# Optimization experiments

Hardware: AMD Instinct MI355X
Metric: run time of the kernel (lower is better)

The kernel has to match this reference:

```python
import jax, jax.numpy as jnp
import numpy as np

HEADS = 8
DIM_HEAD = 64
SCALE = DIM_HEAD ** -0.5


def setup_inputs() -> dict:
    key = jax.random.key(0)
    ks = jax.random.split(key, 6)
    b, n, dim, inner = 8, 1024, 512, HEADS * DIM_HEAD
    return {
        "x": jax.random.normal(ks[0], (b, n, dim), jnp.float32),
        "y": jax.random.normal(ks[1], (b, n, dim), jnp.float32),
        "wq": jax.random.normal(ks[2], (dim, inner), jnp.float32) * 0.02,
        "wkv": jax.random.normal(ks[3], (dim, 2 * inner), jnp.float32) * 0.02,
        "wout": jax.random.normal(ks[4], (inner, dim), jnp.float32) * 0.02,
        "bout": jnp.zeros((dim,), jnp.float32),
    }


def _split_heads(t):
    # [b, n, h*d] -> [b, h, n, d]
    b, n, hd = t.shape
    return t.reshape(b, n, HEADS, DIM_HEAD).transpose(0, 2, 1, 3)


def _merge_heads(t):
    # [b, h, n, d] -> [b, n, h*d]
    b, h, n, d = t.shape
    return t.transpose(0, 2, 1, 3).reshape(b, n, h * d)


def _cross_attn(q_in, kv_in, wq, wkv, wout, bout):
    # queries from q_in, keys/values from kv_in; top-(nk//4) masked softmax attention
    nk = kv_in.shape[1]
    q = _split_heads(q_in @ wq)                     # [b,h,nq,d]
    kv = kv_in @ wkv                                # [b,nk,2*inner]
    k, v = jnp.split(kv, 2, axis=-1)
    k, v = _split_heads(k), _split_heads(v)         # [b,h,nk,d]
    dots = jnp.einsum('bhid,bhjd->bhij', q, k) * SCALE  # [b,h,nq,nk]
    kk = max(nk // 4, 1)
    kth = jax.lax.top_k(dots, kk)[0][..., -1:]      # k-th largest per row
    masked = jnp.where(dots >= kth, dots, -jnp.inf)
    attn = jax.nn.softmax(masked, axis=-1)
    out = jnp.einsum('bhij,bhjd->bhid', attn, v)
    return _merge_heads(out) @ wout + bout


def reference(x, y, wq, wkv, wout, bout):
    out_y = _cross_attn(y, x, wq, wkv, wout, bout)  # y attends to x
    out_x = _cross_attn(x, y, wq, wkv, wout, bout)  # x attends to y
    return (out_x, out_y)
```

## Files before the change

### kernel.cpp

```cpp
#include <hip/hip_runtime.h>
#include <hip/hip_bf16.h>

typedef __attribute__((ext_vector_type(8))) short bfx8;
typedef __attribute__((ext_vector_type(4))) float fx4;

__device__ __forceinline__ short f2bf(float f) {
    union { float f; unsigned u; } v; v.f = f;
    unsigned r = v.u + 0x7fffu + ((v.u >> 16) & 1u);
    return (short)(r >> 16);
}
__device__ __forceinline__ float bf2f(short b) {
    union { unsigned u; float f; } v; v.u = ((unsigned)(unsigned short)b) << 16; return v.f;
}

__global__ __launch_bounds__(256) void proj_kernel(
    const float* __restrict__ X, const float* __restrict__ Y,
    const float* __restrict__ wq, const float* __restrict__ wkv,
    short* __restrict__ QpX, short* __restrict__ KpX, short* __restrict__ VbX,
    short* __restrict__ QpY, short* __restrict__ KpY, short* __restrict__ VbY)
{
    const int inp = blockIdx.z;
    const float* A = inp ? Y : X;
    short* Qp = inp ? QpY : QpX;
    short* Kp = inp ? KpY : KpX;
    short* Vb = inp ? VbY : VbX;
    const int mb = blockIdx.x;
    const int nb = blockIdx.y;
    const int tid = threadIdx.x;
    const int lane = tid & 63;
    const int w = tid >> 6, wm = w >> 1, wn = w & 1;
    const int l15 = lane & 15, g8 = (lane >> 4) * 8;

    __shared__ short As[128][72];
    __shared__ short Bs[128][72];

    const float* Bsrc; int ldb, nbase0;
    if (nb < 4) { Bsrc = wq;  ldb = 512;  nbase0 = nb * 128; }
    else        { Bsrc = wkv; ldb = 1024; nbase0 = nb * 128 - 512; }

    fx4 acc[4][4];
    const fx4 z4 = {0.f, 0.f, 0.f, 0.f};
    for (int i = 0; i < 4; i++) for (int j = 0; j < 4; j++) acc[i][j] = z4;

    const int arow = tid >> 1, ahalf = (tid & 1) * 16;
    const int bk = tid >> 3, bnseg = (tid & 7) * 16;

    for (int kb = 0; kb < 512; kb += 32) {
        __syncthreads();
        {
            const float* src = A + (size_t)(mb * 128 + arow) * 512 + kb + ahalf;
            bfx8 h0, h1, l0, l1;
            #pragma unroll
            for (int q = 0; q < 4; q++) {
                float4 v = *(const float4*)(src + q * 4);
                float vv[4] = {v.x, v.y, v.z, v.w};
                #pragma unroll
                for (int c = 0; c < 4; c++) {
                    int idx = q * 4 + c;
                    short h = f2bf(vv[c]);
                    short l = f2bf(vv[c] - bf2f(h));
                    if (idx < 8) { h0[idx] = h; l0[idx] = l; }
                    else         { h1[idx - 8] = h; l1[idx - 8] = l; }
                }
            }
            *(bfx8*)&As[arow][ahalf] = h0;      *(bfx8*)&As[arow][ahalf + 8] = h1;
            *(bfx8*)&As[arow][32 + ahalf] = l0; *(bfx8*)&As[arow][32 + ahalf + 8] = l1;
        }
        {
            const float* src = Bsrc + (size_t)(kb + bk) * ldb + nbase0 + bnseg;
            #pragma unroll
            for (int q = 0; q < 4; q++) {
                float4 v = *(const float4*)(src + q * 4);
                float vv[4] = {v.x, v.y, v.z, v.w};
                #pragma unroll
                for (int c = 0; c < 4; c++) {
                    int n = bnseg + q * 4 + c;
                    short h = f2bf(vv[c]);
                    Bs[n][bk] = h;
                    Bs[n][32 + bk] = f2bf(vv[c] - bf2f(h));
                }
            }
        }
        __syncthreads();
        bfx8 ah[4], al[4], bh[4], bl[4];
        #pragma unroll
        for (int mt = 0; mt < 4; mt++) {
            int r = wm * 64 + mt * 16 + l15;
            ah[mt] = *(bfx8*)&As[r][g8];
            al[mt] = *(bfx8*)&As[r][32 + g8];
        }
        #pragma unroll
        for (int nt = 0; nt < 4; nt++) {
            int r = wn * 64 + nt * 16 + l15;
            bh[nt] = *(bfx8*)&Bs[r][g8];
            bl[nt] = *(bfx8*)&Bs[r][32 + g8];
        }
        #pragma unroll
        for (int mt = 0; mt < 4; mt++)
            #pragma unroll
            for (int nt = 0; nt < 4; nt++) {
                acc[mt][nt] = __builtin_amdgcn_mfma_f32_16x16x32_bf16(ah[mt], bh[nt], acc[mt][nt], 0, 0, 0);
                acc[mt][nt] = __builtin_amdgcn_mfma_f32_16x16x32_bf16(ah[mt], bl[nt], acc[mt][nt], 0, 0, 0);
                acc[mt][nt] = __builtin_amdgcn_mfma_f32_16x16x32_bf16(al[mt], bh[nt], acc[mt][nt], 0, 0, 0);
            }
    }
    #pragma unroll
    for (int mt = 0; mt < 4; mt++)
        #pragma unroll
        for (int nt = 0; nt < 4; nt++)
            #pragma unroll
            for (int r = 0; r < 4; r++) {
                int row = mb * 128 + wm * 64 + mt * 16 + (lane >> 4) * 4 + r;
                int col = nb * 128 + wn * 64 + nt * 16 + l15;
                float v = acc[mt][nt][r];
                int b = row >> 10, n = row & 1023;
                if (col < 512) {
                    v *= 0.125f;
                    int h = col >> 6, d = col & 63;
                    size_t base = ((size_t)(b * 8 + h) * 1024 + n) * 128;
                    short hi = f2bf(v);
                    Qp[base + d] = hi;
                    Qp[base + 64 + d] = f2bf(v - bf2f(hi));
                } else if (col < 1024) {
                    int cc = col - 512;
                    int h = cc >> 6, d = cc & 63;
                    size_t base = ((size_t)(b * 8 + h) * 1024 + n) * 128;
                    short hi = f2bf(v);
                    Kp[base + d] = hi;
                    Kp[base + 64 + d] = f2bf(v - bf2f(hi));
                } else {
                    Vb[(size_t)row * 512 + (col - 1024)] = f2bf(v);
                }
            }
}

__global__ __launch_bounds__(256) void transv_kernel(
    const short* __restrict__ VbX, const short* __restrict__ VbY,
    short* __restrict__ VtX, short* __restrict__ VtY)
{
    const int inp = blockIdx.z;
    const short* Vb = inp ? VbY : VbX;
    short* Vt = inp ? VtY : VtX;
    const int bh = blockIdx.y, b = bh >> 3, h = bh & 7;
    const int nt = blockIdx.x;
    const int tid = threadIdx.x;
    __shared__ short tile[64][66];
    {
        int r = tid >> 2, c0 = (tid & 3) * 16;
        const short* src = Vb + ((size_t)(b * 1024 + nt * 64 + r)) * 512 + h * 64 + c0;
        bfx8 v0 = *(const bfx8*)src;
        bfx8 v1 = *(const bfx8*)(src + 8);
        #pragma unroll
        for (int i = 0; i < 8; i++) { tile[r][c0 + i] = v0[i]; tile[r][c0 + 8 + i] = v1[i]; }
    }
    __syncthreads();
    {
        int d = tid >> 2, n0 = (tid & 3) * 16;
        bfx8 o0, o1;
        #pragma unroll
        for (int i = 0; i < 8; i++) { o0[i] = tile[n0 + i][d]; o1[i] = tile[n0 + 8 + i][d]; }
        short* dst = Vt + ((size_t)(bh * 64 + d)) * 1024 + nt * 64 + n0;
        *(bfx8*)dst = o0;
        *(bfx8*)(dst + 8) = o1;
    }
}

#define SP 1028
#define ATTN_LDS (131584 + 17408 + 256)

__global__ __launch_bounds__(512) void attn_kernel(
    const short* __restrict__ QpX, const short* __restrict__ KpX, const short* __restrict__ VtX,
    const short* __restrict__ QpY, const short* __restrict__ KpY, const short* __restrict__ VtY,
    short* __restrict__ inner)
{
    extern __shared__ char smem[];
    float* S = (float*)smem;
    short* Kt = (short*)(smem + 131584);
    unsigned* hist = (unsigned*)Kt;
    float* cand = (float*)Kt;
    float* rowinv = (float*)(smem + 131584 + 17408);
    int*   rowcnt = (int*)(smem + 131584 + 17408 + 128);

    const int dir = blockIdx.z;
    const short* Qp = dir ? QpY : QpX;
    const short* Kp = dir ? KpX : KpY;
    const short* Vt = dir ? VtX : VtY;
    const int bh = blockIdx.y;
    const int qb = blockIdx.x;
    const int tid = threadIdx.x;
    const int lane = tid & 63;
    const int widx = tid >> 6;
    const int wm = widx >> 2;
    const int ws = widx & 3;
    const int l15 = lane & 15, g = lane >> 4;

    bfx8 qf[2][2];
    {
        const short* qbase = Qp + ((size_t)bh * 1024 + qb * 32 + wm * 16 + l15) * 128;
        #pragma unroll
        for (int ks = 0; ks < 2; ks++)
            #pragma unroll
            for (int p = 0; p < 2; p++)
                qf[ks][p] = *(const bfx8*)(qbase + p * 64 + ks * 32 + g * 8);
    }

    const int strow = tid >> 3, stseg = (tid & 7) * 16;
    for (int ch = 0; ch < 16; ++ch) {
        __syncthreads();
        {
            const short* src = Kp + ((size_t)bh * 1024 + ch * 64 + strow) * 128 + stseg;
            bfx8 a = *(const bfx8*)src;
            bfx8 b = *(const bfx8*)(src + 8);
            *(bfx8*)&Kt[strow * 136 + stseg] = a;
            *(bfx8*)&Kt[strow * 136 + stseg + 8] = b;
        }
        __syncthreads();
        fx4 acc = {0.f, 0.f, 0.f, 0.f};
        const int krow = ws * 16 + l15;
        #pragma unroll
        for (int ks = 0; ks < 2; ks++) {
            bfx8 kh = *(bfx8*)&Kt[krow * 136 + ks * 32 + g * 8];
            bfx8 kl = *(bfx8*)&Kt[krow * 136 + 64 + ks * 32 + g * 8];
            acc = __builtin_amdgcn_mfma_f32_16x16x32_bf16(qf[ks][0], kh, acc, 0, 0, 0);
            acc = __builtin_amdgcn_mfma_f32_16x16x32_bf16(qf[ks][0], kl, acc, 0, 0, 0);
            acc = __builtin_amdgcn_mfma_f32_16x16x32_bf16(qf[ks][1], kh, acc, 0, 0, 0);
        }
        const int col = ch * 64 + ws * 16 + l15;
        #pragma unroll
        for (int r = 0; r < 4; r++)
            S[(size_t)(wm * 16 + g * 4 + r) * SP + col] = acc[r];
    }
    __syncthreads();
    if (tid < 32) rowcnt[tid] = 0;
    __syncthreads();

    for (int rr = 0; rr < 4; ++rr) {
        const int row = widx * 4 + rr;
        float* Srow = S + (size_t)row * SP;
        float vloc[16];
        #pragma unroll
        for (int i = 0; i < 16; i++) vloc[i] = Srow[lane + 64 * i];
        float mx = -3.4e38f, mn = 3.4e38f;
        #pragma unroll
        for (int i = 0; i < 16; i++) { mx = fmaxf(mx, vloc[i]); mn = fminf(mn, vloc[i]); }
        #pragma unroll
        for (int o = 32; o; o >>= 1) { mx = fmaxf(mx, __shfl_xor(mx, o)); mn = fminf(mn, __shfl_xor(mn, o)); }

        float t;
        if (mx - mn < 1e-30f) {
            t = mx;
        } else {
            const float inv = 128.0f / (mx - mn);
            unsigned* hrow = hist + row * 128;
            hrow[lane] = 0; hrow[lane + 64] = 0;
            #pragma unroll
            for (int i = 0; i < 16; i++) {
                int bin = (int)((vloc[i] - mn) * inv);
                bin = bin > 127 ? 127 : (bin < 0 ? 0 : bin);
                atomicAdd(&hrow[bin], 1u);
            }
            unsigned c0 = hrow[2 * lane], c1 = hrow[2 * lane + 1];
            unsigned ts = c0 + c1;
            #pragma unroll
            for (int o = 1; o < 64; o <<= 1) {
                unsigned u = __shfl_down(ts, o);
                if (lane + o < 64) ts += u;
            }
            unsigned ca_lo = ts - c0;
            unsigned ca_hi = ts - c0 - c1;
            bool oklo = (ca_lo < 256u) && (ca_lo + c0 >= 256u);
            bool okhi = (ca_hi < 256u) && (ca_hi + c1 >= 256u);
            unsigned long long bal = __ballot(oklo || okhi);
            int sl = __ffsll((long long)bal) - 1;
            int myB = oklo ? 2 * lane : 2 * lane + 1;
            int myCA = (int)(oklo ? ca_lo : ca_hi);
            int B = __shfl(myB, sl);
            int need = 256 - __shfl(myCA, sl);
            float* crow = cand + row * 128;
            #pragma unroll
            for (int i = 0; i < 16; i++) {
                int bin = (int)((vloc[i] - mn) * inv);
                bin = bin > 127 ? 127 : (bin < 0 ? 0 : bin);
                if (bin == B) {
                    int idx = atomicAdd(&rowcnt[row], 1);
                    if (idx < 128) crow[idx] = vloc[i];
                }
            }
            int m = rowcnt[row]; m = m > 128 ? 128 : m;
            float v0 = (lane < m) ? crow[lane] : 0.f;
            float v1 = (lane + 64 < m) ? crow[lane + 64] : 0.f;
            int cg0 = 0, ce0 = 0, cg1 = 0, ce1 = 0;
            for (int i = 0; i < m; i++) {
                float c = crow[i];
                cg0 += c > v0; ce0 += c == v0;
                cg1 += c > v1; ce1 += c == v1;
            }
            bool ok0 = (lane < m) && (cg0 < need) && (need <= cg0 + ce0);
            bool ok1 = (lane + 64 < m) && (cg1 < need) && (need <= cg1 + ce1);
            unsigned long long b0 = __ballot(ok0);
            unsigned long long b1 = __ballot(ok1);
            if (b0)      t = __shfl(v0, __ffsll((long long)b0) - 1);
            else if (b1) t = __shfl(v1, __ffsll((long long)b1) - 1);
            else         t = mx;
        }
        float sum = 0.f;
        short ploc[16];
        #pragma unroll
        for (int i = 0; i < 16; i++) {
            float p = (vloc[i] >= t) ? expf(vloc[i] - mx) : 0.f;
            sum += p;
            ploc[i] = f2bf(p);
        }
        #pragma unroll
        for (int o = 32; o; o >>= 1) sum += __shfl_xor(sum, o);
        short* Prow = (short*)Srow;
        #pragma unroll
        for (int i = 0; i < 16; i++) Prow[lane + 64 * i] = ploc[i];
        if (lane == 0) rowinv[row] = 1.0f / sum;
    }
    __syncthreads();

    {
        const int wd = ws;
        const short* vrow = Vt + ((size_t)bh * 64 + wd * 16 + l15) * 1024;
        const short* Prow = (const short*)(S + (size_t)(wm * 16 + l15) * SP);
        fx4 acc0 = {0.f, 0.f, 0.f, 0.f}, acc1 = {0.f, 0.f, 0.f, 0.f};
        #pragma unroll 4
        for (int ks = 0; ks < 32; ks += 2) {
            bfx8 pa0 = *(const bfx8*)&Prow[ks * 32 + g * 8];
            bfx8 vv0 = *(const bfx8*)(vrow + ks * 32 + g * 8);
            bfx8 pa1 = *(const bfx8*)&Prow[(ks + 1) * 32 + g * 8];
            bfx8 vv1 = *(const bfx8*)(vrow + (ks + 1) * 32 + g * 8);
            acc0 = __builtin_amdgcn_mfma_f32_16x16x32_bf16(pa0, vv0, acc0, 0, 0, 0);
            acc1 = __builtin_amdgcn_mfma_f32_16x16x32_bf16(pa1, vv1, acc1, 0, 0, 0);
        }
        #pragma unroll
        for (int r = 0; r < 4; r++) {
            int qrow = wm * 16 + g * 4 + r;
            float v = (acc0[r] + acc1[r]) * rowinv[qrow];
            size_t orow = (size_t)dir * 8192 + (size_t)(bh >> 3) * 1024 + qb * 32 + qrow;
            inner[orow * 512 + (bh & 7) * 64 + wd * 16 + l15] = f2bf(v);
        }
    }
}

__global__ __launch_bounds__(256) void outproj_kernel(
    const short* __restrict__ inner, const float* __restrict__ wout,
    const float* __restrict__ bout, float* __restrict__ out)
{
    const int mb = blockIdx.x;
    const int nb = blockIdx.y;
    const int tid = threadIdx.x;
    const int lane = tid & 63;
    const int w = tid >> 6, wm = w >> 1, wn = w & 1;
    const int l15 = lane & 15, g8 = (lane >> 4) * 8;

    __shared__ short As[128][40];
    __shared__ short Bs[128][40];

    fx4 acc[4][4];
    const fx4 z4 = {0.f, 0.f, 0.f, 0.f};
    for (int i = 0; i < 4; i++) for (int j = 0; j < 4; j++) acc[i][j] = z4;

    const int arow = tid >> 1, ahalf = (tid & 1) * 16;
    const int bk = tid >> 3, bnseg = (tid & 7) * 16;

    for (int kb = 0; kb < 512; kb += 32) {
        __syncthreads();
        {
            const short* src = inner + (size_t)(mb * 128 + arow) * 512 + kb + ahalf;
            bfx8 v0 = *(const bfx8*)src, v1 = *(const bfx8*)(src + 8);
            *(bfx8*)&As[arow][ahalf] = v0;
            *(bfx8*)&As[arow][ahalf + 8] = v1;
        }
        {
            const float* src = wout + (size_t)(kb + bk) * 512 + nb * 128 + bnseg;
            #pragma unroll
            for (int q = 0; q < 4; q++) {
                float4 v = *(const float4*)(src + q * 4);
                float vv[4] = {v.x, v.y, v.z, v.w};
                #pragma unroll
                for (int c = 0; c < 4; c++) Bs[bnseg + q * 4 + c][bk] = f2bf(vv[c]);
            }
        }
        __syncthreads();
        bfx8 af[4], bf[4];
        #pragma unroll
        for (int mt = 0; mt < 4; mt++) af[mt] = *(bfx8*)&As[wm * 64 + mt * 16 + l15][g8];
        #pragma unroll
        for (int nt = 0; nt < 4; nt++) bf[nt] = *(bfx8*)&Bs[wn * 64 + nt * 16 + l15][g8];
        #pragma unroll
        for (int mt = 0; mt < 4; mt++)
            #pragma unroll
            for (int nt = 0; nt < 4; nt++)
                acc[mt][nt] = __builtin_amdgcn_mfma_f32_16x16x32_bf16(af[mt], bf[nt], acc[mt][nt], 0, 0, 0);
    }
    #pragma unroll
    for (int mt = 0; mt < 4; mt++)
        #pragma unroll
        for (int nt = 0; nt < 4; nt++)
            #pragma unroll
            for (int r = 0; r < 4; r++) {
                int row = mb * 128 + wm * 64 + mt * 16 + (lane >> 4) * 4 + r;
                int col = nb * 128 + wn * 64 + nt * 16 + l15;
                out[(size_t)row * 512 + col] = acc[mt][nt][r] + bout[col];
            }
}

extern "C" void kernel_launch(void* const* d_in, const int* in_sizes, int n_in,
                              void* d_out, int out_size, void* d_ws, size_t ws_size,
                              hipStream_t stream)
{
    const float* x    = (const float*)d_in[0];
    const float* y    = (const float*)d_in[1];
    const float* wq   = (const float*)d_in[2];
    const float* wkv  = (const float*)d_in[3];
    const float* wout = (const float*)d_in[4];
    const float* bout = (const float*)d_in[5];
    float* out = (float*)d_out;

    char* ws = (char*)d_ws;
    size_t off = 0;
    auto alloc = [&](size_t bytes) -> void* {
        void* p = ws + off; off += (bytes + 255) & ~(size_t)255; return p;
    };
    const size_t QP = (size_t)8 * 8 * 1024 * 128 * 2;
    const size_t VB = (size_t)8192 * 512 * 2;
    short* QpX = (short*)alloc(QP);
    short* KpX = (short*)alloc(QP);
    short* QpY = (short*)alloc(QP);
    short* KpY = (short*)alloc(QP);
    short* VbX = (short*)alloc(VB);
    short* VbY = (short*)alloc(VB);
    short* VtX = (short*)alloc(VB);
    short* VtY = (short*)alloc(VB);
    short* inner = (short*)alloc((size_t)2 * 8192 * 512 * 2);
    if (off > ws_size) return;

    proj_kernel<<<dim3(64, 12, 2), 256, 0, stream>>>(x, y, wq, wkv, QpX, KpX, VbX, QpY, KpY, VbY);
    transv_kernel<<<dim3(16, 64, 2), 256, 0, stream>>>(VbX, VbY, VtX, VtY);
    (void)hipFuncSetAttribute((const void*)attn_kernel,
                              hipFuncAttributeMaxDynamicSharedMemorySize, ATTN_LDS);
    attn_kernel<<<dim3(32, 64, 2), 512, ATTN_LDS, stream>>>(QpX, KpX, VtX, QpY, KpY, VtY, inner);
    outproj_kernel<<<dim3(128, 4, 1), 256, 0, stream>>>(inner, wout, bout, out);
}
```

Measured before the change: 847.2 us.

## Keep attention scores in registers and compute top-k threshold block-wide

The QK^T scores now stay in MFMA accumulator registers (16 tiles per wave, each wave owning a 256-key slice) instead of going through a 128KB fp32 LDS score buffer with per-chunk K staging and barriers. Row max/min, the histogram (now 96 bins) and candidate collection are done cooperatively across waves through small LDS partial arrays. Only bf16 probabilities are written to a swizzled 64KB LDS buffer, so occupancy can rise (launch_bounds 512,4). The costs are much higher register pressure, more block barriers, __expf instead of expf, and a changed threshold fallback when candidates overflow the 64-entry buffer.

```diff
diff --git a/kernel.cpp b/kernel.cpp
--- a/kernel.cpp
+++ b/kernel.cpp
@@ -165,21 +165,36 @@
     }
 }
 
-#define SP 1028
-#define ATTN_LDS (131584 + 17408 + 256)
-
-__global__ __launch_bounds__(512) void attn_kernel(
+#define PBUF_OFF 0
+#define HIST_OFF 65536
+#define PMX_OFF  77824
+#define PMN_OFF  78336
+#define PSUM_OFF 78848
+#define RMX_OFF  79360
+#define RMN_OFF  79488
+#define RT_OFF   79616
+#define RB_OFF   79744
+#define RN_OFF   79872
+#define RC_OFF   80000
+#define ATTN_LDS 80128
+
+__global__ __launch_bounds__(512, 4) void attn_kernel(
     const short* __restrict__ QpX, const short* __restrict__ KpX, const short* __restrict__ VtX,
     const short* __restrict__ QpY, const short* __restrict__ KpY, const short* __restrict__ VtY,
     short* __restrict__ inner)
 {
     extern __shared__ char smem[];
-    float* S = (float*)smem;
-    short* Kt = (short*)(smem + 131584);
-    unsigned* hist = (unsigned*)Kt;
-    float* cand = (float*)Kt;
-    float* rowinv = (float*)(smem + 131584 + 17408);
-    int*   rowcnt = (int*)(smem + 131584 + 17408 + 128);
+    unsigned* histU  = (unsigned*)(smem + HIST_OFF);
+    float*    candF  = (float*)(smem + HIST_OFF);
+    float*    partmx = (float*)(smem + PMX_OFF);
+    float*    partmn = (float*)(smem + PMN_OFF);
+    float*    partsum= (float*)(smem + PSUM_OFF);
+    float*    rowMx  = (float*)(smem + RMX_OFF);
+    float*    rowMn  = (float*)(smem + RMN_OFF);
+    float*    rowT   = (float*)(smem + RT_OFF);
+    int*      rowB   = (int*)(smem + RB_OFF);
+    int*      rowNeed= (int*)(smem + RN_OFF);
+    int*      rowcnt = (int*)(smem + RC_OFF);
 
     const int dir = blockIdx.z;
     const short* Qp = dir ? QpY : QpX;
@@ -204,132 +219,177 @@
                 qf[ks][p] = *(const bfx8*)(qbase + p * 64 + ks * 32 + g * 8);
     }
 
-    const int strow = tid >> 3, stseg = (tid & 7) * 16;
-    for (int ch = 0; ch < 16; ++ch) {
-        __syncthreads();
-        {
-            const short* src = Kp + ((size_t)bh * 1024 + ch * 64 + strow) * 128 + stseg;
-            bfx8 a = *(const bfx8*)src;
-            bfx8 b = *(const bfx8*)(src + 8);
-            *(bfx8*)&Kt[strow * 136 + stseg] = a;
-            *(bfx8*)&Kt[strow * 136 + stseg + 8] = b;
-        }
-        __syncthreads();
-        fx4 acc = {0.f, 0.f, 0.f, 0.f};
-        const int krow = ws * 16 + l15;
-        #pragma unroll
-        for (int ks = 0; ks < 2; ks++) {
-            bfx8 kh = *(bfx8*)&Kt[krow * 136 + ks * 32 + g * 8];
-            bfx8 kl = *(bfx8*)&Kt[krow * 136 + 64 + ks * 32 + g * 8];
-            acc = __builtin_amdgcn_mfma_f32_16x16x32_bf16(qf[ks][0], kh, acc, 0, 0, 0);
-            acc = __builtin_amdgcn_mfma_f32_16x16x32_bf16(qf[ks][0], kl, acc, 0, 0, 0);
-            acc = __builtin_amdgcn_mfma_f32_16x16x32_bf16(qf[ks][1], kh, acc, 0, 0, 0);
-        }
-        const int col = ch * 64 + ws * 16 + l15;
-        #pragma unroll
-        for (int r = 0; r < 4; r++)
-            S[(size_t)(wm * 16 + g * 4 + r) * SP + col] = acc[r];
-    }
-    __syncthreads();
+    fx4 acc[16];
+    {
+        const fx4 z4 = {0.f, 0.f, 0.f, 0.f};
+        #pragma unroll
+        for (int t = 0; t < 16; t++) acc[t] = z4;
+        const short* kbase = Kp + ((size_t)bh * 1024 + ws * 256 + l15) * 128 + g * 8;
+        #pragma unroll
+        for (int t = 0; t < 16; t++) {
+            const short* kb = kbase + (size_t)t * 16 * 128;
+            bfx8 kh0 = *(const bfx8*)(kb);
+            bfx8 kh1 = *(const bfx8*)(kb + 32);
+            bfx8 kl0 = *(const bfx8*)(kb + 64);
+            bfx8 kl1 = *(const bfx8*)(kb + 96);
+            acc[t] = __builtin_amdgcn_mfma_f32_16x16x32_bf16(qf[0][0], kh0, acc[t], 0, 0, 0);
+            acc[t] = __builtin_amdgcn_mfma_f32_16x16x32_bf16(qf[0][0], kl0, acc[t], 0, 0, 0);
+            acc[t] = __builtin_amdgcn_mfma_f32_16x16x32_bf16(qf[0][1], kh0, acc[t], 0, 0, 0);
+            acc[t] = __builtin_amdgcn_mfma_f32_16x16x32_bf16(qf[1][0], kh1, acc[t], 0, 0, 0);
+            acc[t] = __builtin_amdgcn_mfma_f32_16x16x32_bf16(qf[1][0], kl1, acc[t], 0, 0, 0);
+            acc[t] = __builtin_amdgcn_mfma_f32_16x16x32_bf16(qf[1][1], kh1, acc[t], 0, 0, 0);
+        }
+    }
+
+    float rmx[4], rmn[4];
+    #pragma unroll
+    for (int r = 0; r < 4; r++) {
+        float a = acc[0][r], b = acc[0][r];
+        #pragma unroll
+        for (int t = 1; t < 16; t++) { a = fmaxf(a, acc[t][r]); b = fminf(b, acc[t][r]); }
+        #pragma unroll
+        for (int o = 1; o < 16; o <<= 1) { a = fmaxf(a, __shfl_xor(a, o)); b = fminf(b, __shfl_xor(b, o)); }
+        rmx[r] = a; rmn[r] = b;
+    }
+    if (l15 == 0) {
+        #pragma unroll
+        for (int r = 0; r < 4; r++) {
+            int lrow = wm * 16 + g * 4 + r;
+            partmx[lrow * 4 + ws] = rmx[r];
+            partmn[lrow * 4 + ws] = rmn[r];
+        }
+    }
+    for (int i = tid; i < 32 * 96; i += 512) histU[i] = 0;
     if (tid < 32) rowcnt[tid] = 0;
     __syncthreads();
 
-    for (int rr = 0; rr < 4; ++rr) {
-        const int row = widx * 4 + rr;
-        float* Srow = S + (size_t)row * SP;
-        float vloc[16];
-        #pragma unroll
-        for (int i = 0; i < 16; i++) vloc[i] = Srow[lane + 64 * i];
-        float mx = -3.4e38f, mn = 3.4e38f;
-        #pragma unroll
-        for (int i = 0; i < 16; i++) { mx = fmaxf(mx, vloc[i]); mn = fminf(mn, vloc[i]); }
-        #pragma unroll
-        for (int o = 32; o; o >>= 1) { mx = fmaxf(mx, __shfl_xor(mx, o)); mn = fminf(mn, __shfl_xor(mn, o)); }
-
-        float t;
-        if (mx - mn < 1e-30f) {
-            t = mx;
-        } else {
-            const float inv = 128.0f / (mx - mn);
-            unsigned* hrow = hist + row * 128;
-            hrow[lane] = 0; hrow[lane + 64] = 0;
-            #pragma unroll
-            for (int i = 0; i < 16; i++) {
-                int bin = (int)((vloc[i] - mn) * inv);
-                bin = bin > 127 ? 127 : (bin < 0 ? 0 : bin);
-                atomicAdd(&hrow[bin], 1u);
-            }
-            unsigned c0 = hrow[2 * lane], c1 = hrow[2 * lane + 1];
-            unsigned ts = c0 + c1;
-            #pragma unroll
-            for (int o = 1; o < 64; o <<= 1) {
-                unsigned u = __shfl_down(ts, o);
-                if (lane + o < 64) ts += u;
-            }
-            unsigned ca_lo = ts - c0;
-            unsigned ca_hi = ts - c0 - c1;
-            bool oklo = (ca_lo < 256u) && (ca_lo + c0 >= 256u);
-            bool okhi = (ca_hi < 256u) && (ca_hi + c1 >= 256u);
-            unsigned long long bal = __ballot(oklo || okhi);
-            int sl = __ffsll((long long)bal) - 1;
-            int myB = oklo ? 2 * lane : 2 * lane + 1;
-            int myCA = (int)(oklo ? ca_lo : ca_hi);
-            int B = __shfl(myB, sl);
-            int need = 256 - __shfl(myCA, sl);
-            float* crow = cand + row * 128;
-            #pragma unroll
-            for (int i = 0; i < 16; i++) {
-                int bin = (int)((vloc[i] - mn) * inv);
-                bin = bin > 127 ? 127 : (bin < 0 ? 0 : bin);
-                if (bin == B) {
-                    int idx = atomicAdd(&rowcnt[row], 1);
-                    if (idx < 128) crow[idx] = vloc[i];
-                }
-            }
-            int m = rowcnt[row]; m = m > 128 ? 128 : m;
-            float v0 = (lane < m) ? crow[lane] : 0.f;
-            float v1 = (lane + 64 < m) ? crow[lane + 64] : 0.f;
-            int cg0 = 0, ce0 = 0, cg1 = 0, ce1 = 0;
-            for (int i = 0; i < m; i++) {
-                float c = crow[i];
-                cg0 += c > v0; ce0 += c == v0;
-                cg1 += c > v1; ce1 += c == v1;
-            }
-            bool ok0 = (lane < m) && (cg0 < need) && (need <= cg0 + ce0);
-            bool ok1 = (lane + 64 < m) && (cg1 < need) && (need <= cg1 + ce1);
-            unsigned long long b0 = __ballot(ok0);
-            unsigned long long b1 = __ballot(ok1);
-            if (b0)      t = __shfl(v0, __ffsll((long long)b0) - 1);
-            else if (b1) t = __shfl(v1, __ffsll((long long)b1) - 1);
-            else         t = mx;
-        }
-        float sum = 0.f;
-        short ploc[16];
-        #pragma unroll
-        for (int i = 0; i < 16; i++) {
-            float p = (vloc[i] >= t) ? expf(vloc[i] - mx) : 0.f;
-            sum += p;
-            ploc[i] = f2bf(p);
-        }
-        #pragma unroll
-        for (int o = 32; o; o >>= 1) sum += __shfl_xor(sum, o);
-        short* Prow = (short*)Srow;
-        #pragma unroll
-        for (int i = 0; i < 16; i++) Prow[lane + 64 * i] = ploc[i];
-        if (lane == 0) rowinv[row] = 1.0f / sum;
+    float mxr[4], mnr[4], invr[4];
+    #pragma unroll
+    for (int r = 0; r < 4; r++) {
+        int lrow = wm * 16 + g * 4 + r;
+        float a = partmx[lrow * 4 + 0], b = partmn[lrow * 4 + 0];
+        #pragma unroll
+        for (int j = 1; j < 4; j++) { a = fmaxf(a, partmx[lrow * 4 + j]); b = fminf(b, partmn[lrow * 4 + j]); }
+        mxr[r] = a; mnr[r] = b;
+        invr[r] = (a - b > 1e-30f) ? 96.0f / (a - b) : 0.0f;
+    }
+    if (ws == 0 && l15 == 0) {
+        #pragma unroll
+        for (int r = 0; r < 4; r++) {
+            int lrow = wm * 16 + g * 4 + r;
+            rowMx[lrow] = mxr[r]; rowMn[lrow] = mnr[r];
+        }
+    }
+    #pragma unroll
+    for (int r = 0; r < 4; r++) {
+        int lrow = wm * 16 + g * 4 + r;
+        #pragma unroll
+        for (int t = 0; t < 16; t++) {
+            int bin = (int)((acc[t][r] - mnr[r]) * invr[r]);
+            bin = bin < 0 ? 0 : (bin > 95 ? 95 : bin);
+            atomicAdd(&histU[lrow * 96 + bin], 1u);
+        }
+    }
+    __syncthreads();
+
+    #pragma unroll
+    for (int rr = 0; rr < 4; rr++) {
+        int row = widx * 4 + rr;
+        unsigned c0 = 0, c1 = 0;
+        if (lane < 48) { c0 = histU[row * 96 + 2 * lane]; c1 = histU[row * 96 + 2 * lane + 1]; }
+        unsigned ts = c0 + c1;
+        #pragma unroll
+        for (int o = 1; o < 64; o <<= 1) {
+            unsigned u = __shfl_down(ts, o);
+            if (lane + o < 64) ts += u;
+        }
+        unsigned ca_lo = ts - c0, ca_hi = ts - c0 - c1;
+        bool oklo = (lane < 48) && (ca_lo < 256u) && (ca_lo + c0 >= 256u);
+        bool okhi = (lane < 48) && (ca_hi < 256u) && (ca_hi + c1 >= 256u);
+        unsigned long long bal = __ballot(oklo || okhi);
+        int sl = __ffsll((long long)bal) - 1;
+        int myB = oklo ? 2 * lane : 2 * lane + 1;
+        int myNeed = 256 - (int)(oklo ? ca_lo : ca_hi);
+        int B = __shfl(myB, sl);
+        int need = __shfl(myNeed, sl);
+        if (lane == 0) {
+            float mr = rowMx[row], nr = rowMn[row];
+            if (mr - nr < 1e-30f) { rowB[row] = -1; rowT[row] = nr; rowNeed[row] = 1; }
+            else { rowB[row] = B; rowNeed[row] = need; }
+        }
+    }
+    __syncthreads();
+
+    #pragma unroll
+    for (int r = 0; r < 4; r++) {
+        int lrow = wm * 16 + g * 4 + r;
+        int B = rowB[lrow];
+        #pragma unroll
+        for (int t = 0; t < 16; t++) {
+            int bin = (int)((acc[t][r] - mnr[r]) * invr[r]);
+            bin = bin < 0 ? 0 : (bin > 95 ? 95 : bin);
+            if (B >= 0 && bin == B) {
+                int idx = atomicAdd(&rowcnt[lrow], 1);
+                if (idx < 64) candF[lrow * 64 + idx] = acc[t][r];
+            }
+        }
+    }
+    __syncthreads();
+
+    #pragma unroll
+    for (int rr = 0; rr < 4; rr++) {
+        int row = widx * 4 + rr;
+        int B = rowB[row];
+        if (B < 0) continue;
+        int m = rowcnt[row]; m = m > 64 ? 64 : m;
+        int need = rowNeed[row];
+        const float* crow = candF + row * 64;
+        float v0 = (lane < m) ? crow[lane] : 0.f;
+        int cg = 0, ce = 0;
+        for (int i = 0; i < m; i++) {
+            float c = crow[i];
+            cg += (c > v0); ce += (c == v0);
+        }
+        bool ok = (lane < m) && (cg < need) && (need <= cg + ce);
+        unsigned long long bal = __ballot(ok);
+        float tt;
+        if (bal) tt = __shfl(v0, __ffsll((long long)bal) - 1);
+        else     tt = rowMn[row] + (float)B * (rowMx[row] - rowMn[row]) * (1.0f / 96.0f);
+        if (lane == 0) rowT[row] = tt;
+    }
+    __syncthreads();
+
+    #pragma unroll
+    for (int r = 0; r < 4; r++) {
+        int lrow = wm * 16 + g * 4 + r;
+        float tthr = rowT[lrow];
+        float s = 0.f;
+        unsigned sw = (unsigned)((lrow & 7) << 4);
+        #pragma unroll
+        for (int t = 0; t < 16; t++) {
+            float v = acc[t][r];
+            float p = (v >= tthr) ? __expf(v - mxr[r]) : 0.f;
+            s += p;
+            int col = ws * 256 + t * 16 + l15;
+            *(short*)(smem + (size_t)lrow * 2048 + (((unsigned)(col * 2)) ^ sw)) = f2bf(p);
+        }
+        #pragma unroll
+        for (int o = 1; o < 16; o <<= 1) s += __shfl_xor(s, o);
+        if (l15 == 0) partsum[lrow * 4 + ws] = s;
     }
     __syncthreads();
 
     {
-        const int wd = ws;
-        const short* vrow = Vt + ((size_t)bh * 64 + wd * 16 + l15) * 1024;
-        const short* Prow = (const short*)(S + (size_t)(wm * 16 + l15) * SP);
+        const short* vrow = Vt + ((size_t)bh * 64 + ws * 16 + l15) * 1024;
+        const int arow = wm * 16 + l15;
+        const unsigned sw = (unsigned)((arow & 7) << 4);
+        const char* pbase = smem + (size_t)arow * 2048;
         fx4 acc0 = {0.f, 0.f, 0.f, 0.f}, acc1 = {0.f, 0.f, 0.f, 0.f};
-        #pragma unroll 4
+        #pragma unroll
         for (int ks = 0; ks < 32; ks += 2) {
-            bfx8 pa0 = *(const bfx8*)&Prow[ks * 32 + g * 8];
+            bfx8 pa0 = *(const bfx8*)(pbase + (((unsigned)(ks * 64 + g * 16)) ^ sw));
             bfx8 vv0 = *(const bfx8*)(vrow + ks * 32 + g * 8);
-            bfx8 pa1 = *(const bfx8*)&Prow[(ks + 1) * 32 + g * 8];
+            bfx8 pa1 = *(const bfx8*)(pbase + (((unsigned)((ks + 1) * 64 + g * 16)) ^ sw));
             bfx8 vv1 = *(const bfx8*)(vrow + (ks + 1) * 32 + g * 8);
             acc0 = __builtin_amdgcn_mfma_f32_16x16x32_bf16(pa0, vv0, acc0, 0, 0, 0);
             acc1 = __builtin_amdgcn_mfma_f32_16x16x32_bf16(pa1, vv1, acc1, 0, 0, 0);
@@ -337,9 +397,11 @@
         #pragma unroll
         for (int r = 0; r < 4; r++) {
             int qrow = wm * 16 + g * 4 + r;
-            float v = (acc0[r] + acc1[r]) * rowinv[qrow];
+            float inv = 1.0f / (partsum[qrow * 4 + 0] + partsum[qrow * 4 + 1] +
+                                partsum[qrow * 4 + 2] + partsum[qrow * 4 + 3]);
+            float v = (acc0[r] + acc1[r]) * inv;
             size_t orow = (size_t)dir * 8192 + (size_t)(bh >> 3) * 1024 + qb * 32 + qrow;
-            inner[orow * 512 + (bh & 7) * 64 + wd * 16 + l15] = f2bf(v);
+            inner[orow * 512 + (bh & 7) * 64 + ws * 16 + l15] = f2bf(v);
         }
     }
 }
```

Result: no change. 836.9 us (-1.2%).
